# Performance work log

Measured on AMD Instinct MI355X. Metric: run time of the kernel, lower is better.

Reference implementation:

```python
import jax, jax.numpy as jnp
import numpy as np

# ---- Cl(3,0) Cayley table, basis order [1, e1, e2, e3, e12, e13, e23, e123] ----
def _build_cayley():
    order = [0b000, 0b001, 0b010, 0b100, 0b011, 0b101, 0b110, 0b111]
    idx = {m: i for i, m in enumerate(order)}
    M = np.zeros((8, 8, 8), np.float32)
    for i, a in enumerate(order):
        for j, b in enumerate(order):
            aa, swaps = a >> 1, 0
            while aa:
                swaps += bin(aa & b).count('1')
                aa >>= 1
            M[i, j, idx[a ^ b]] = -1.0 if (swaps % 2) else 1.0
    return M

CAYLEY = jnp.asarray(_build_cayley())  # (8,8,8): c_k = a_i b_j M[i,j,k]

B, D, H, R, K = 16384, 512, 256, 95, 8

def _layernorm(x, g, b, eps=1e-5):
    mu = jnp.mean(x, axis=-1, keepdims=True)
    var = jnp.var(x, axis=-1, keepdims=True)
    return (x - mu) * jax.lax.rsqrt(var + eps) * g + b

def _proj(h, W1, b1, lg, lb, W2, b2):
    x = h @ W1 + b1
    x = _layernorm(x, lg, lb)
    x = jax.nn.gelu(x, approximate=False)  # torch nn.GELU default = exact erf
    return (x @ W2 + b2).reshape(h.shape[0], K, 8)  # dropout is eval-mode identity

def setup_inputs() -> dict:
    key = jax.random.key(0)
    ks = jax.random.split(key, 16)
    s1, s2 = 1.0 / np.sqrt(D), 1.0 / np.sqrt(H)
    inp = {
        'h_perp': jax.random.normal(ks[0], (B, D), jnp.float32),
        'h_vuln': jax.random.normal(ks[1], (B, D), jnp.float32),
        'Wp1': jax.random.normal(ks[2], (D, H), jnp.float32) * s1,
        'bp1': jnp.zeros((H,), jnp.float32),
        'lgp': jnp.ones((H,), jnp.float32),
        'lbp': jnp.zeros((H,), jnp.float32),
        'Wp2': jax.random.normal(ks[3], (H, K * 8), jnp.float32) * s2,
        'bp2': jnp.zeros((K * 8,), jnp.float32),
        'Wv1': jax.random.normal(ks[4], (D, H), jnp.float32) * s1,
        'bv1': jnp.zeros((H,), jnp.float32),
        'lgv': jnp.ones((H,), jnp.float32),
        'lbv': jnp.zeros((H,), jnp.float32),
        'Wv2': jax.random.normal(ks[5], (H, K * 8), jnp.float32) * s2,
        'bv2': jnp.zeros((K * 8,), jnp.float32),
        'T': jax.random.normal(ks[6], (R, K, 8), jnp.float32) * 0.1,
        'gw': jnp.zeros((8,), jnp.float32).at[0].set(1.0),
    }
    return inp

def reference(h_perp, h_vuln, Wp1, bp1, lgp, lbp, Wp2, bp2,
              Wv1, bv1, lgv, lbv, Wv2, bv2, T, gw):
    m_perp = _proj(h_perp, Wp1, bp1, lgp, lbp, Wp2, bp2)  # (B,K,8)
    m_vuln = _proj(h_vuln, Wv1, bv1, lgv, lbv, Wv2, bv2)  # (B,K,8)
    # triple product: (m_perp x T_r) x m_vuln  via Cayley tensor
    at = jnp.einsum('bki,rkj,ijm->brkm', m_perp, T, CAYLEY)          # (B,R,K,8)
    res = jnp.einsum('brkm,bkj,mjn->brkn', at, m_vuln, CAYLEY)       # (B,R,K,8)
    weighted = jnp.einsum('brkn,n->brk', res, gw)                    # grade-weighted readout
    return jnp.mean(weighted, axis=-1)                               # (B,R) logits
```

## Files before the change

### kernel.cpp

```cpp
#include <hip/hip_runtime.h>
#include <math.h>


#define B_ 16384
#define D_ 512
#define H_ 256
#define R_ 95

typedef __attribute__((ext_vector_type(8))) short short8;
typedef __attribute__((ext_vector_type(4))) float f32x4;

#define MFMA(a, b, c) __builtin_amdgcn_mfma_f32_16x16x32_bf16(a, b, c, 0, 0, 0)

__device__ __forceinline__ short f2bf(float x) {
    union { float f; unsigned u; } v; v.f = x;
    unsigned r = v.u + 0x7fffu + ((v.u >> 16) & 1u);
    return (short)(r >> 16);
}
__device__ __forceinline__ float bf2f(short s) {
    union { float f; unsigned u; } v;
    v.u = ((unsigned)(unsigned short)s) << 16;
    return v.f;
}

__device__ __forceinline__ float gelu_fast(float x) {
    const float z  = x * 0.70710678118654752f;
    const float az = fabsf(z);
    const float t  = 1.0f / fmaf(0.3275911f, az, 1.0f);
    float p = fmaf(1.061405429f, t, -1.453152027f);
    p = fmaf(p, t, 1.421413741f);
    p = fmaf(p, t, -0.284496736f);
    p = fmaf(p, t, 0.254829592f);
    p *= t;
    const float e  = 1.0f - p * __expf(-az * az);
    const float er = copysignf(e, z);
    return 0.5f * x * (1.0f + er);
}

__global__ __launch_bounds__(256)
void cdd_prep_kernel(const float* __restrict__ Wp1, const float* __restrict__ Wv1,
                     const float* __restrict__ Wp2, const float* __restrict__ Wv2,
                     short* __restrict__ W1c_p, short* __restrict__ W1c_v,
                     short* __restrict__ W2t_p, short* __restrict__ W2t_v)
{
    const int o = blockIdx.x * 256 + threadIdx.x;
    if (o < 16 * 256 * 32) {
        const int n = o & 255, kin = (o >> 8) & 31, ch = o >> 13;
        const int src = (ch * 32 + kin) * 256 + n;
        const int dst = ch * 8192 + n * 32 + kin;
        W1c_p[dst] = f2bf(Wp1[src]);
        W1c_v[dst] = f2bf(Wv1[src]);
    }
    if (o < 64 * 256) {
        const int n = o >> 8, k = o & 255;
        W2t_p[o] = f2bf(Wp2[k * 64 + n]);
        W2t_v[o] = f2bf(Wv2[k * 64 + n]);
    }
}

__global__ __launch_bounds__(256, 2)
void cdd_proj_kernel(const float* __restrict__ h_p, const float* __restrict__ h_v,
                     const float* __restrict__ bp1, const float* __restrict__ lgp,
                     const float* __restrict__ lbp, const float* __restrict__ bp2,
                     const float* __restrict__ bv1, const float* __restrict__ lgv,
                     const float* __restrict__ lbv, const float* __restrict__ bv2,
                     const short* __restrict__ W1c_p, const short* __restrict__ W1c_v,
                     const short* __restrict__ W2t_p, const short* __restrict__ W2t_v,
                     short* __restrict__ mp_out, short* __restrict__ mv_out)
{
    __shared__ __align__(16) short hs[32 * 512];
    __shared__ __align__(16) short xs[32 * 264];
    __shared__ __align__(16) float lnbuf[256];

    const int which = blockIdx.y;
    const float* __restrict__ h   = which ? h_v : h_p;
    const float* __restrict__ b1  = which ? bv1 : bp1;
    const float* __restrict__ lg  = which ? lgv : lgp;
    const float* __restrict__ lb  = which ? lbv : lbp;
    const float* __restrict__ b2  = which ? bv2 : bp2;
    const short* __restrict__ W1c = which ? W1c_v : W1c_p;
    const short* __restrict__ W2t = which ? W2t_v : W2t_p;
    short* __restrict__ mo = which ? mv_out : mp_out;

    const int t = threadIdx.x;
    const int w = t >> 6, l = t & 63, q = l >> 4, c = l & 15;
    const int b0 = blockIdx.x * 32;

    {
        const int row = t >> 3, kbase = (t & 7) * 64;
        const int mt_s = row >> 4, c_s = row & 15;
        const float* hrp = h + (size_t)(b0 + row) * D_ + kbase;
#pragma unroll
        for (int s = 0; s < 8; ++s) {
            const float4 u0 = *(const float4*)(hrp + s * 8);
            const float4 u1 = *(const float4*)(hrp + s * 8 + 4);
            short8 pk;
            pk[0] = f2bf(u0.x); pk[1] = f2bf(u0.y); pk[2] = f2bf(u0.z); pk[3] = f2bf(u0.w);
            pk[4] = f2bf(u1.x); pk[5] = f2bf(u1.y); pk[6] = f2bf(u1.z); pk[7] = f2bf(u1.w);
            const int k0 = kbase + s * 8;
            const int ch = k0 >> 5, qd = (k0 & 31) >> 3;
            *(short8*)(hs + (ch * 2 + mt_s) * 512 + (qd * 16 + c_s) * 8) = pk;
        }
    }
    __syncthreads();

    f32x4 acc1[2][4];
#pragma unroll
    for (int mt = 0; mt < 2; ++mt)
#pragma unroll
        for (int nt = 0; nt < 4; ++nt) acc1[mt][nt] = 0;

    const short* Wb0 = W1c + (w * 64 + c) * 32 + q * 8;
    short8 wb0[4], wb1[4];
#pragma unroll
    for (int nt = 0; nt < 4; ++nt) wb0[nt] = *(const short8*)(Wb0 + nt * 512);

#pragma unroll 1
    for (int cp = 0; cp < 8; ++cp) {
        const int ch0 = cp * 2, ch1 = cp * 2 + 1;
#pragma unroll
        for (int nt = 0; nt < 4; ++nt)
            wb1[nt] = *(const short8*)(Wb0 + ch1 * 8192 + nt * 512);
        {
            const short8 a0 = *(const short8*)(hs + (ch0 * 2 + 0) * 512 + l * 8);
            const short8 a1 = *(const short8*)(hs + (ch0 * 2 + 1) * 512 + l * 8);
#pragma unroll
            for (int nt = 0; nt < 4; ++nt) {
                acc1[0][nt] = MFMA(a0, wb0[nt], acc1[0][nt]);
                acc1[1][nt] = MFMA(a1, wb0[nt], acc1[1][nt]);
            }
        }
        if (cp < 7) {
#pragma unroll
            for (int nt = 0; nt < 4; ++nt)
                wb0[nt] = *(const short8*)(Wb0 + (ch0 + 2) * 8192 + nt * 512);
        }
        {
            const short8 a0 = *(const short8*)(hs + (ch1 * 2 + 0) * 512 + l * 8);
            const short8 a1 = *(const short8*)(hs + (ch1 * 2 + 1) * 512 + l * 8);
#pragma unroll
            for (int nt = 0; nt < 4; ++nt) {
                acc1[0][nt] = MFMA(a0, wb1[nt], acc1[0][nt]);
                acc1[1][nt] = MFMA(a1, wb1[nt], acc1[1][nt]);
            }
        }
    }

    float bb[4], gg[4], ee[4];
#pragma unroll
    for (int nt = 0; nt < 4; ++nt) {
        const int col = w * 64 + nt * 16 + c;
        bb[nt] = b1[col]; gg[nt] = lg[col]; ee[nt] = lb[col];
    }
    float mean[2][4], rstd[2][4];
#pragma unroll
    for (int mt = 0; mt < 2; ++mt)
#pragma unroll
        for (int reg = 0; reg < 4; ++reg) {
            float s1 = 0.f, s2 = 0.f;
#pragma unroll
            for (int nt = 0; nt < 4; ++nt) {
                const float a = acc1[mt][nt][reg] + bb[nt];
                acc1[mt][nt][reg] = a;
                s1 += a; s2 += a * a;
            }
#pragma unroll
            for (int m = 1; m <= 8; m <<= 1) {
                s1 += __shfl_xor(s1, m, 64);
                s2 += __shfl_xor(s2, m, 64);
            }
            if (c == 0) {
                const int row = mt * 16 + q * 4 + reg;
                *(float2*)(lnbuf + (w * 32 + row) * 2) = make_float2(s1, s2);
            }
        }
    __syncthreads();
#pragma unroll
    for (int mt = 0; mt < 2; ++mt)
#pragma unroll
        for (int reg = 0; reg < 4; ++reg) {
            const int row = mt * 16 + q * 4 + reg;
            float S1 = 0.f, S2 = 0.f;
#pragma unroll
            for (int w2 = 0; w2 < 4; ++w2) {
                const float2 p = *(const float2*)(lnbuf + (w2 * 32 + row) * 2);
                S1 += p.x; S2 += p.y;
            }
            const float mu = S1 * (1.f / 256.f);
            const float var = S2 * (1.f / 256.f) - mu * mu;
            mean[mt][reg] = mu;
            rstd[mt][reg] = rsqrtf(var + 1e-5f);
        }
#pragma unroll
    for (int mt = 0; mt < 2; ++mt)
#pragma unroll
        for (int reg = 0; reg < 4; ++reg) {
            const int row = mt * 16 + q * 4 + reg;
            const float mu = mean[mt][reg], rs = rstd[mt][reg];
#pragma unroll
            for (int nt = 0; nt < 4; ++nt) {
                const int col = w * 64 + nt * 16 + c;
                const float xv = (acc1[mt][nt][reg] - mu) * rs * gg[nt] + ee[nt];
                xs[row * 264 + col] = f2bf(gelu_fast(xv));
            }
        }
    __syncthreads();

    f32x4 acc2[2]; acc2[0] = 0; acc2[1] = 0;
    const short* W2b = W2t + (w * 16 + c) * 256 + q * 8;
#pragma unroll
    for (int ks = 0; ks < 8; ++ks) {
        const short8 xa0 = *(const short8*)(xs + c * 264 + ks * 32 + q * 8);
        const short8 xa1 = *(const short8*)(xs + (16 + c) * 264 + ks * 32 + q * 8);
        const short8 wbk = *(const short8*)(W2b + ks * 32);
        acc2[0] = MFMA(xa0, wbk, acc2[0]);
        acc2[1] = MFMA(xa1, wbk, acc2[1]);
    }
    const float bc = b2[w * 16 + c];
#pragma unroll
    for (int mt = 0; mt < 2; ++mt)
#pragma unroll
        for (int reg = 0; reg < 4; ++reg) {
            const int row = mt * 16 + q * 4 + reg;
            mo[(size_t)(b0 + row) * 64 + w * 16 + c] = f2bf(acc2[mt][reg] + bc);
        }
}

__global__ __launch_bounds__(256, 2)
void cdd_cliff_kernel(const short* __restrict__ mp, const short* __restrict__ mv,
                      const float* __restrict__ T, const float* __restrict__ gw,
                      float* __restrict__ out)
{
    __shared__ __align__(16) float wfl[32 * 68];
    __shared__ __align__(16) float ts[95 * 68];
    const int t  = threadIdx.x;
    const int b0 = blockIdx.x * 32;

#pragma unroll
    for (int k = 0; k < 6; ++k) {
        const int o = t + k * 256;
        if (o < 95 * 16) {
            const int rr = o >> 4, c4 = (o & 15) << 2;
            *(float4*)(ts + rr * 68 + c4) = *(const float4*)(T + rr * 64 + c4);
        }
    }

    {
        const int row = t >> 3, kq = t & 7;
        float g[8];
#pragma unroll
        for (int i = 0; i < 8; ++i) g[i] = gw[i];
        const short8 p8 = *(const short8*)(mp + (size_t)(b0 + row) * 64 + kq * 8);
        const short8 q8 = *(const short8*)(mv + (size_t)(b0 + row) * 64 + kq * 8);
        float mpv[8], mvv[8];
#pragma unroll
        for (int i = 0; i < 8; ++i) { mpv[i] = bf2f(p8[i]); mvv[i] = bf2f(q8[i]); }

        constexpr int MSK[8] = {0, 1, 2, 4, 3, 5, 6, 7};
        float v[8];
#pragma unroll
        for (int m = 0; m < 8; ++m) {
            float s = 0.f;
#pragma unroll
            for (int j = 0; j < 8; ++j) {
                const int am = MSK[m], bm = MSK[j];
                const int par = (__popc((am >> 1) & bm) + __popc((am >> 2) & bm)) & 1;
                const float sg = par ? -1.f : 1.f;
                s = fmaf(sg * g[MSK[am ^ bm]], mvv[j], s);
            }
            v[m] = s;
        }
#pragma unroll
        for (int l2 = 0; l2 < 8; ++l2) {
            float s = 0.f;
#pragma unroll
            for (int i = 0; i < 8; ++i) {
                const int am = MSK[i], bm = MSK[l2];
                const int par = (__popc((am >> 1) & bm) + __popc((am >> 2) & bm)) & 1;
                const float sg = par ? -1.f : 1.f;
                s = fmaf(sg * mpv[i], v[MSK[am ^ bm]], s);
            }
            wfl[row * 68 + kq * 8 + l2] = s;
        }
    }
    __syncthreads();

    {
        const int rr = t >> 3, rl = t & 7;
        float4 wv[16];
#pragma unroll
        for (int cc = 0; cc < 16; ++cc)
            wv[cc] = *(const float4*)(wfl + rr * 68 + cc * 4);
#pragma unroll
        for (int k = 0; k < 12; ++k) {
            const int r = rl + (k << 3);
            if (r < R_) {
                float s = 0.f;
#pragma unroll
                for (int cc = 0; cc < 16; ++cc) {
                    const float4 tv = *(const float4*)(ts + r * 68 + cc * 4);
                    s += wv[cc].x * tv.x + wv[cc].y * tv.y
                       + wv[cc].z * tv.z + wv[cc].w * tv.w;
                }
                out[(size_t)(b0 + rr) * R_ + r] = 0.125f * s;
            }
        }
    }
}

extern "C" void kernel_launch(void* const* d_in, const int* in_sizes, int n_in,
                              void* d_out, int out_size, void* d_ws, size_t ws_size,
                              hipStream_t stream)
{
    const float* h_p = (const float*)d_in[0];
    const float* h_v = (const float*)d_in[1];
    const float* Wp1 = (const float*)d_in[2];
    const float* bp1 = (const float*)d_in[3];
    const float* lgp = (const float*)d_in[4];
    const float* lbp = (const float*)d_in[5];
    const float* Wp2 = (const float*)d_in[6];
    const float* bp2 = (const float*)d_in[7];
    const float* Wv1 = (const float*)d_in[8];
    const float* bv1 = (const float*)d_in[9];
    const float* lgv = (const float*)d_in[10];
    const float* lbv = (const float*)d_in[11];
    const float* Wv2 = (const float*)d_in[12];
    const float* bv2 = (const float*)d_in[13];
    const float* T   = (const float*)d_in[14];
    const float* gw  = (const float*)d_in[15];
    float* out = (float*)d_out;

    short* W1c_p = (short*)d_ws;
    short* W1c_v = W1c_p + 16 * 256 * 32;
    short* W2t_p = W1c_v + 16 * 256 * 32;
    short* W2t_v = W2t_p + 64 * 256;
    short* mp    = W2t_v + 64 * 256;
    short* mv    = mp + (size_t)B_ * 64;

    cdd_prep_kernel<<<512, 256, 0, stream>>>(Wp1, Wv1, Wp2, Wv2,
                                             W1c_p, W1c_v, W2t_p, W2t_v);
    dim3 g1(B_ / 32, 2);
    cdd_proj_kernel<<<g1, 256, 0, stream>>>(h_p, h_v,
                                            bp1, lgp, lbp, bp2,
                                            bv1, lgv, lbv, bv2,
                                            W1c_p, W1c_v, W2t_p, W2t_v,
                                            mp, mv);
    cdd_cliff_kernel<<<B_ / 32, 256, 0, stream>>>(mp, mv, T, gw, out);
}
```

Measured before the change: 163.8 us.

## Double rows per projection block and stage input in two K halves

Each projection block now handles 64 batch rows instead of 32. Every W1 fragment loaded from global memory is reused across four M tiles instead of two, which halves total W1 traffic and the number of blocks. To keep LDS usage the same, the h input is converted and staged in two 256-column halves with a sync between them. The trade-off is more accumulator registers (16 acc tiles) and less overlap between loading h and issuing MFMAs, so occupancy and latency hiding may drop.

```diff
diff --git a/kernel.cpp b/kernel.cpp
--- a/kernel.cpp
+++ b/kernel.cpp
@@ -68,9 +68,9 @@
                      const short* __restrict__ W2t_p, const short* __restrict__ W2t_v,
                      short* __restrict__ mp_out, short* __restrict__ mv_out)
 {
-    __shared__ __align__(16) short hs[32 * 512];
-    __shared__ __align__(16) short xs[32 * 264];
-    __shared__ __align__(16) float lnbuf[256];
+    __shared__ __align__(16) short hs[64 * 256];
+    __shared__ __align__(16) short xs[64 * 264];
+    __shared__ __align__(16) float lnbuf[512];
 
     const int which = blockIdx.y;
     const float* __restrict__ h   = which ? h_v : h_p;
@@ -84,29 +84,13 @@
 
     const int t = threadIdx.x;
     const int w = t >> 6, l = t & 63, q = l >> 4, c = l & 15;
-    const int b0 = blockIdx.x * 32;
-
-    {
-        const int row = t >> 3, kbase = (t & 7) * 64;
-        const int mt_s = row >> 4, c_s = row & 15;
-        const float* hrp = h + (size_t)(b0 + row) * D_ + kbase;
-#pragma unroll
-        for (int s = 0; s < 8; ++s) {
-            const float4 u0 = *(const float4*)(hrp + s * 8);
-            const float4 u1 = *(const float4*)(hrp + s * 8 + 4);
-            short8 pk;
-            pk[0] = f2bf(u0.x); pk[1] = f2bf(u0.y); pk[2] = f2bf(u0.z); pk[3] = f2bf(u0.w);
-            pk[4] = f2bf(u1.x); pk[5] = f2bf(u1.y); pk[6] = f2bf(u1.z); pk[7] = f2bf(u1.w);
-            const int k0 = kbase + s * 8;
-            const int ch = k0 >> 5, qd = (k0 & 31) >> 3;
-            *(short8*)(hs + (ch * 2 + mt_s) * 512 + (qd * 16 + c_s) * 8) = pk;
-        }
-    }
-    __syncthreads();
-
-    f32x4 acc1[2][4];
-#pragma unroll
-    for (int mt = 0; mt < 2; ++mt)
+    const int b0 = blockIdx.x * 64;
+    const int srow = t >> 2, kseg = (t & 3) * 64;
+    const int mt_s = srow >> 4, c_s = srow & 15;
+
+    f32x4 acc1[4][4];
+#pragma unroll
+    for (int mt = 0; mt < 4; ++mt)
 #pragma unroll
         for (int nt = 0; nt < 4; ++nt) acc1[mt][nt] = 0;
 
@@ -115,34 +99,42 @@
 #pragma unroll
     for (int nt = 0; nt < 4; ++nt) wb0[nt] = *(const short8*)(Wb0 + nt * 512);
 
-#pragma unroll 1
-    for (int cp = 0; cp < 8; ++cp) {
-        const int ch0 = cp * 2, ch1 = cp * 2 + 1;
-#pragma unroll
-        for (int nt = 0; nt < 4; ++nt)
-            wb1[nt] = *(const short8*)(Wb0 + ch1 * 8192 + nt * 512);
+    for (int kh = 0; kh < 2; ++kh) {
+        if (kh) __syncthreads();
         {
-            const short8 a0 = *(const short8*)(hs + (ch0 * 2 + 0) * 512 + l * 8);
-            const short8 a1 = *(const short8*)(hs + (ch0 * 2 + 1) * 512 + l * 8);
-#pragma unroll
-            for (int nt = 0; nt < 4; ++nt) {
-                acc1[0][nt] = MFMA(a0, wb0[nt], acc1[0][nt]);
-                acc1[1][nt] = MFMA(a1, wb0[nt], acc1[1][nt]);
-            }
-        }
-        if (cp < 7) {
-#pragma unroll
-            for (int nt = 0; nt < 4; ++nt)
-                wb0[nt] = *(const short8*)(Wb0 + (ch0 + 2) * 8192 + nt * 512);
-        }
-        {
-            const short8 a0 = *(const short8*)(hs + (ch1 * 2 + 0) * 512 + l * 8);
-            const short8 a1 = *(const short8*)(hs + (ch1 * 2 + 1) * 512 + l * 8);
-#pragma unroll
-            for (int nt = 0; nt < 4; ++nt) {
-                acc1[0][nt] = MFMA(a0, wb1[nt], acc1[0][nt]);
-                acc1[1][nt] = MFMA(a1, wb1[nt], acc1[1][nt]);
-            }
+            const float* hrp = h + (size_t)(b0 + srow) * D_ + kh * 256 + kseg;
+#pragma unroll
+            for (int s = 0; s < 8; ++s) {
+                const float4 u0 = *(const float4*)(hrp + s * 8);
+                const float4 u1 = *(const float4*)(hrp + s * 8 + 4);
+                short8 pk;
+                pk[0] = f2bf(u0.x); pk[1] = f2bf(u0.y); pk[2] = f2bf(u0.z); pk[3] = f2bf(u0.w);
+                pk[4] = f2bf(u1.x); pk[5] = f2bf(u1.y); pk[6] = f2bf(u1.z); pk[7] = f2bf(u1.w);
+                const int kk = kseg + s * 8;
+                const int ch = kk >> 5, qd = (kk >> 3) & 3;
+                *(short8*)(hs + (ch * 4 + mt_s) * 512 + (qd * 16 + c_s) * 8) = pk;
+            }
+        }
+        __syncthreads();
+
+        for (int ch = 0; ch < 8; ++ch) {
+            const int g = kh * 8 + ch;
+            if (g < 15) {
+#pragma unroll
+                for (int nt = 0; nt < 4; ++nt)
+                    wb1[nt] = *(const short8*)(Wb0 + (g + 1) * 8192 + nt * 512);
+            }
+            short8 a[4];
+#pragma unroll
+            for (int mt = 0; mt < 4; ++mt)
+                a[mt] = *(const short8*)(hs + (ch * 4 + mt) * 512 + l * 8);
+#pragma unroll
+            for (int mt = 0; mt < 4; ++mt)
+#pragma unroll
+                for (int nt = 0; nt < 4; ++nt)
+                    acc1[mt][nt] = MFMA(a[mt], wb0[nt], acc1[mt][nt]);
+#pragma unroll
+            for (int nt = 0; nt < 4; ++nt) wb0[nt] = wb1[nt];
         }
     }
 
@@ -152,9 +144,8 @@
         const int col = w * 64 + nt * 16 + c;
         bb[nt] = b1[col]; gg[nt] = lg[col]; ee[nt] = lb[col];
     }
-    float mean[2][4], rstd[2][4];
-#pragma unroll
-    for (int mt = 0; mt < 2; ++mt)
+#pragma unroll
+    for (int mt = 0; mt < 4; ++mt)
 #pragma unroll
         for (int reg = 0; reg < 4; ++reg) {
             float s1 = 0.f, s2 = 0.f;
@@ -171,32 +162,24 @@
             }
             if (c == 0) {
                 const int row = mt * 16 + q * 4 + reg;
-                *(float2*)(lnbuf + (w * 32 + row) * 2) = make_float2(s1, s2);
+                *(float2*)(lnbuf + (w * 64 + row) * 2) = make_float2(s1, s2);
             }
         }
     __syncthreads();
 #pragma unroll
-    for (int mt = 0; mt < 2; ++mt)
+    for (int mt = 0; mt < 4; ++mt)
 #pragma unroll
         for (int reg = 0; reg < 4; ++reg) {
             const int row = mt * 16 + q * 4 + reg;
             float S1 = 0.f, S2 = 0.f;
 #pragma unroll
             for (int w2 = 0; w2 < 4; ++w2) {
-                const float2 p = *(const float2*)(lnbuf + (w2 * 32 + row) * 2);
+                const float2 p = *(const float2*)(lnbuf + (w2 * 64 + row) * 2);
                 S1 += p.x; S2 += p.y;
             }
-            const float mu = S1 * (1.f / 256.f);
+            const float mu  = S1 * (1.f / 256.f);
             const float var = S2 * (1.f / 256.f) - mu * mu;
-            mean[mt][reg] = mu;
-            rstd[mt][reg] = rsqrtf(var + 1e-5f);
-        }
-#pragma unroll
-    for (int mt = 0; mt < 2; ++mt)
-#pragma unroll
-        for (int reg = 0; reg < 4; ++reg) {
-            const int row = mt * 16 + q * 4 + reg;
-            const float mu = mean[mt][reg], rs = rstd[mt][reg];
+            const float rs  = rsqrtf(var + 1e-5f);
 #pragma unroll
             for (int nt = 0; nt < 4; ++nt) {
                 const int col = w * 64 + nt * 16 + c;
@@ -206,19 +189,22 @@
         }
     __syncthreads();
 
-    f32x4 acc2[2]; acc2[0] = 0; acc2[1] = 0;
+    f32x4 acc2[4];
+#pragma unroll
+    for (int mt = 0; mt < 4; ++mt) acc2[mt] = 0;
     const short* W2b = W2t + (w * 16 + c) * 256 + q * 8;
 #pragma unroll
     for (int ks = 0; ks < 8; ++ks) {
-        const short8 xa0 = *(const short8*)(xs + c * 264 + ks * 32 + q * 8);
-        const short8 xa1 = *(const short8*)(xs + (16 + c) * 264 + ks * 32 + q * 8);
         const short8 wbk = *(const short8*)(W2b + ks * 32);
-        acc2[0] = MFMA(xa0, wbk, acc2[0]);
-        acc2[1] = MFMA(xa1, wbk, acc2[1]);
+#pragma unroll
+        for (int mt = 0; mt < 4; ++mt) {
+            const short8 xa = *(const short8*)(xs + (mt * 16 + c) * 264 + ks * 32 + q * 8);
+            acc2[mt] = MFMA(xa, wbk, acc2[mt]);
+        }
     }
     const float bc = b2[w * 16 + c];
 #pragma unroll
-    for (int mt = 0; mt < 2; ++mt)
+    for (int mt = 0; mt < 4; ++mt)
 #pragma unroll
         for (int reg = 0; reg < 4; ++reg) {
             const int row = mt * 16 + q * 4 + reg;
@@ -339,7 +325,7 @@
 
     cdd_prep_kernel<<<512, 256, 0, stream>>>(Wp1, Wv1, Wp2, Wv2,
                                              W1c_p, W1c_v, W2t_p, W2t_v);
-    dim3 g1(B_ / 32, 2);
+    dim3 g1(B_ / 64, 2);
     cdd_proj_kernel<<<g1, 256, 0, stream>>>(h_p, h_v,
                                             bp1, lgp, lbp, bp2,
                                             bv1, lgv, lbv, bv2,
```

Result: faster. 158.9 us (-3.0%).
